# Kernel tuning notes

Hardware: AMD Instinct MI355X
Metric: run time of the kernel (lower is better)

The kernel has to match this reference:

```python
import jax, jax.numpy as jnp
import numpy as np

KERNEL = 128
STRIDE = 64


def setup_inputs() -> dict:
    key = jax.random.key(0)
    k1, k2, k3 = jax.random.split(key, 3)
    in_features = 8192
    fold_num = (in_features - KERNEL) // STRIDE + 1  # 127
    local_features = 128
    batch = 2048
    x = jax.random.normal(k1, (batch, in_features), dtype=jnp.float32)
    # stacked per-window Linear weights/biases (PyTorch Linear: y = x @ W.T + b)
    bound = 1.0 / np.sqrt(KERNEL)
    W = jax.random.uniform(k2, (fold_num, local_features, KERNEL), dtype=jnp.float32,
                           minval=-bound, maxval=bound)
    b = jax.random.uniform(k3, (fold_num, local_features), dtype=jnp.float32,
                           minval=-bound, maxval=bound)
    return {"x": x, "W": W, "b": b}


def reference(x, W, b):
    fold_num = W.shape[0]
    # window gather indices: [fold_num, kernel]
    idx = STRIDE * jnp.arange(fold_num)[:, None] + jnp.arange(KERNEL)[None, :]
    windows = x[:, idx]                      # [batch, fold_num, kernel]
    # per-window linear: out[b,f,l] = sum_k windows[b,f,k] * W[f,l,k] + b[f,l]
    out = jnp.einsum('bfk,flk->bfl', windows, W) + b[None, :, :]
    # concat along feature dim as in torch.cat(..., 1)
    return out.reshape(out.shape[0], -1)     # [batch, fold_num*local_features]
```

## Files before the change

kernel.cpp:

```cpp
#include <hip/hip_runtime.h>
#include <hip/hip_bf16.h>

typedef float f32x4 __attribute__((ext_vector_type(4)));
typedef __bf16 bf16x8 __attribute__((ext_vector_type(8)));

#define INF   8192
#define FOLDS 127
#define LOCAL 128
#define OUTF  (FOLDS * LOCAL)
#define BM    128

#define WB_BYTES ((size_t)FOLDS * LOCAL * 128 * 2)

__global__ void convert_w_kernel(const float* __restrict__ W, __bf16* __restrict__ Wb) {
    const size_t i = ((size_t)blockIdx.x * 256 + threadIdx.x) * 8;
    f32x4 v0 = *(const f32x4*)(W + i);
    f32x4 v1 = *(const f32x4*)(W + i + 4);
    bf16x8 w;
    w[0] = (__bf16)v0[0]; w[1] = (__bf16)v0[1]; w[2] = (__bf16)v0[2]; w[3] = (__bf16)v0[3];
    w[4] = (__bf16)v1[0]; w[5] = (__bf16)v1[1]; w[6] = (__bf16)v1[2]; w[7] = (__bf16)v1[3];
    *(bf16x8*)(Wb + i) = w;
}

__device__ __forceinline__ void cvt_store8(char* lds, int byte, f32x4 v0, f32x4 v1) {
    bf16x8 w;
    w[0] = (__bf16)v0[0]; w[1] = (__bf16)v0[1]; w[2] = (__bf16)v0[2]; w[3] = (__bf16)v0[3];
    w[4] = (__bf16)v1[0]; w[5] = (__bf16)v1[1]; w[6] = (__bf16)v1[2]; w[7] = (__bf16)v1[3];
    *(bf16x8*)(lds + byte) = w;
}

template<bool WBF16>
__global__ __launch_bounds__(256, 2)
void local_linear_kernel(const float* __restrict__ x,
                         const float* __restrict__ Wf32,
                         const __bf16* __restrict__ Wbf,
                         const float* __restrict__ bias,
                         float* __restrict__ out)
{
    __shared__ __align__(16) __bf16 As[128 * 192];
    __shared__ __align__(16) __bf16 Bs[128 * 128];

    const int mt = blockIdx.x;
    const int fg = blockIdx.y;
    const int f0 = fg * 2;
    const bool has_f1 = (f0 + 1) < FOLDS;
    const int t  = threadIdx.x;

    const int m0 = mt * BM;
    const float* __restrict__ xg = x + (size_t)m0 * INF + (size_t)f0 * 64;

    const int lane = t & 63;
    const int wid  = t >> 6;
    const int wm   = wid >> 1;
    const int wn   = wid & 1;
    const int r16  = lane & 15;
    const int kq   = lane >> 4;

    auto stageB = [&](int f) {
        if constexpr (WBF16) {
            const char* Wsrc = (const char*)(Wbf + (size_t)f * LOCAL * 128);
            #pragma unroll
            for (int c = 0; c < 8; ++c) {
                const int base  = wid * 8192 + c * 1024;
                const int b     = base + lane * 16;
                const int row   = b >> 8;
                const int inner = b & 255;
                const int srcb  = row * 256 + (inner ^ ((row & 7) << 4));
                __builtin_amdgcn_global_load_lds(
                    (const __attribute__((address_space(1))) void*)(Wsrc + srcb),
                    (__attribute__((address_space(3))) void*)((char*)Bs + base),
                    16, 0, 0);
            }
        } else {
            const float* Wf = Wf32 + (size_t)f * LOCAL * 128;
            #pragma unroll
            for (int it = 0; it < 8; ++it) {
                const int e = it * 2048 + t * 8;
                const int row = e >> 7, col = e & 127;
                const float* g = Wf + row * 128 + col;
                f32x4 v0 = *(const f32x4*)g;
                f32x4 v1 = *(const f32x4*)(g + 4);
                cvt_store8((char*)Bs, (row * 256 + col * 2) ^ ((row & 7) << 4), v0, v1);
            }
        }
    };

    stageB(f0);

    #pragma unroll
    for (int it = 0; it < 8; ++it) {
        const int e = it * 2048 + t * 8;
        const int row = e >> 7, col = e & 127;
        const float* g = xg + (size_t)row * INF + col;
        f32x4 v0 = *(const f32x4*)g;
        f32x4 v1 = *(const f32x4*)(g + 4);
        cvt_store8((char*)As, (row * 384 + col * 2) ^ ((row & 7) << 4), v0, v1);
    }
    if (has_f1) {
        #pragma unroll
        for (int it = 0; it < 4; ++it) {
            const int e = it * 2048 + t * 8;
            const int row = e >> 6, col = 128 + (e & 63);
            const float* g = xg + (size_t)row * INF + col;
            f32x4 v0 = *(const f32x4*)g;
            f32x4 v1 = *(const f32x4*)(g + 4);
            cvt_store8((char*)As, (row * 384 + col * 2) ^ ((row & 7) << 4), v0, v1);
        }
    }

    auto computeFold = [&](int f, int acolBase) {
        f32x4 acc[4][4];
        #pragma unroll
        for (int i = 0; i < 4; ++i)
            #pragma unroll
            for (int j = 0; j < 4; ++j)
                acc[i][j] = (f32x4){0.f, 0.f, 0.f, 0.f};

        #pragma unroll
        for (int ks = 0; ks < 4; ++ks) {
            const int kof = ks * 32 + kq * 8;
            bf16x8 a[4], b[4];
            #pragma unroll
            for (int i = 0; i < 4; ++i) {
                const int row  = wm * 64 + i * 16 + r16;
                const int byte = (row * 384 + (acolBase + kof) * 2) ^ ((row & 7) << 4);
                a[i] = *(const bf16x8*)((const char*)As + byte);
            }
            #pragma unroll
            for (int j = 0; j < 4; ++j) {
                const int row  = wn * 64 + j * 16 + r16;
                const int byte = (row * 256 + kof * 2) ^ ((row & 7) << 4);
                b[j] = *(const bf16x8*)((const char*)Bs + byte);
            }
            #pragma unroll
            for (int i = 0; i < 4; ++i)
                #pragma unroll
                for (int j = 0; j < 4; ++j)
                    acc[i][j] = __builtin_amdgcn_mfma_f32_16x16x32_bf16(a[i], b[j], acc[i][j], 0, 0, 0);
        }

        float bv[4];
        #pragma unroll
        for (int j = 0; j < 4; ++j)
            bv[j] = bias[f * LOCAL + wn * 64 + j * 16 + r16];

        #pragma unroll
        for (int i = 0; i < 4; ++i) {
            const int mrow = m0 + wm * 64 + i * 16 + kq * 4;
            #pragma unroll
            for (int j = 0; j < 4; ++j) {
                const int ncol = f * LOCAL + wn * 64 + j * 16 + r16;
                float* o = out + (size_t)mrow * OUTF + ncol;
                #pragma unroll
                for (int r = 0; r < 4; ++r)
                    o[(size_t)r * OUTF] = acc[i][j][r] + bv[j];
            }
        }
    };

    __syncthreads();
    computeFold(f0, 0);

    if (has_f1) {
        __syncthreads();
        stageB(f0 + 1);
        __syncthreads();
        computeFold(f0 + 1, 64);
    }
}

extern "C" void kernel_launch(void* const* d_in, const int* in_sizes, int n_in,
                              void* d_out, int out_size, void* d_ws, size_t ws_size,
                              hipStream_t stream) {
    const float* x    = (const float*)d_in[0];
    const float* W    = (const float*)d_in[1];
    const float* bias = (const float*)d_in[2];
    float* out        = (float*)d_out;

    dim3 grid(2048 / BM, 64);
    dim3 block(256);

    if (ws_size >= WB_BYTES) {
        __bf16* Wb = (__bf16*)d_ws;
        convert_w_kernel<<<1016, 256, 0, stream>>>(W, Wb);
        local_linear_kernel<true><<<grid, block, 0, stream>>>(x, W, Wb, bias, out);
    } else {
        local_linear_kernel<false><<<grid, block, 0, stream>>>(x, W, nullptr, bias, out);
    }
}
```

Before: 50.06 us.

## Assign one fold per block with 512 threads and nontemporal output stores

Each block now handles a single fold instead of two folds sequentially, with 8 waves splitting the 128x128 output tile into 4x2 wave tiles. The grid grows to 16x127 blocks. The bias is folded into the accumulator initialisation, and output stores become nontemporal. This removes the serial second-fold stage and its extra barriers and raises parallelism and occupancy. In exchange, the overlapping x window is loaded twice (once per adjacent fold) instead of being shared between the two folds of a block.

```diff
diff --git a/kernel.cpp b/kernel.cpp
--- a/kernel.cpp
+++ b/kernel.cpp
@@ -30,142 +30,113 @@
 }
 
 template<bool WBF16>
-__global__ __launch_bounds__(256, 2)
+__global__ __launch_bounds__(512, 4)
 void local_linear_kernel(const float* __restrict__ x,
                          const float* __restrict__ Wf32,
                          const __bf16* __restrict__ Wbf,
                          const float* __restrict__ bias,
                          float* __restrict__ out)
 {
-    __shared__ __align__(16) __bf16 As[128 * 192];
+    __shared__ __align__(16) __bf16 As[128 * 128];
     __shared__ __align__(16) __bf16 Bs[128 * 128];
 
     const int mt = blockIdx.x;
-    const int fg = blockIdx.y;
-    const int f0 = fg * 2;
-    const bool has_f1 = (f0 + 1) < FOLDS;
+    const int f  = blockIdx.y;
     const int t  = threadIdx.x;
 
-    const int m0 = mt * BM;
-    const float* __restrict__ xg = x + (size_t)m0 * INF + (size_t)f0 * 64;
-
+    const int m0   = mt * BM;
     const int lane = t & 63;
     const int wid  = t >> 6;
-    const int wm   = wid >> 1;
-    const int wn   = wid & 1;
+    const int wm   = wid >> 2;
+    const int wn   = wid & 3;
     const int r16  = lane & 15;
     const int kq   = lane >> 4;
 
-    auto stageB = [&](int f) {
-        if constexpr (WBF16) {
-            const char* Wsrc = (const char*)(Wbf + (size_t)f * LOCAL * 128);
-            #pragma unroll
-            for (int c = 0; c < 8; ++c) {
-                const int base  = wid * 8192 + c * 1024;
-                const int b     = base + lane * 16;
-                const int row   = b >> 8;
-                const int inner = b & 255;
-                const int srcb  = row * 256 + (inner ^ ((row & 7) << 4));
-                __builtin_amdgcn_global_load_lds(
-                    (const __attribute__((address_space(1))) void*)(Wsrc + srcb),
-                    (__attribute__((address_space(3))) void*)((char*)Bs + base),
-                    16, 0, 0);
-            }
-        } else {
-            const float* Wf = Wf32 + (size_t)f * LOCAL * 128;
-            #pragma unroll
-            for (int it = 0; it < 8; ++it) {
-                const int e = it * 2048 + t * 8;
-                const int row = e >> 7, col = e & 127;
-                const float* g = Wf + row * 128 + col;
-                f32x4 v0 = *(const f32x4*)g;
-                f32x4 v1 = *(const f32x4*)(g + 4);
-                cvt_store8((char*)Bs, (row * 256 + col * 2) ^ ((row & 7) << 4), v0, v1);
-            }
+    if constexpr (WBF16) {
+        const char* Wsrc = (const char*)(Wbf + (size_t)f * LOCAL * 128);
+        #pragma unroll
+        for (int c = 0; c < 4; ++c) {
+            const int base  = wid * 4096 + c * 1024;
+            const int b     = base + lane * 16;
+            const int row   = b >> 8;
+            const int inner = b & 255;
+            const int srcb  = row * 256 + (inner ^ ((row & 7) << 4));
+            __builtin_amdgcn_global_load_lds(
+                (const __attribute__((address_space(1))) void*)(Wsrc + srcb),
+                (__attribute__((address_space(3))) void*)((char*)Bs + base),
+                16, 0, 0);
         }
-    };
+    } else {
+        const float* Wf = Wf32 + (size_t)f * LOCAL * 128;
+        #pragma unroll
+        for (int it = 0; it < 4; ++it) {
+            const int e = it * 4096 + t * 8;
+            const int row = e >> 7, col = e & 127;
+            const float* g = Wf + row * 128 + col;
+            f32x4 v0 = *(const f32x4*)g;
+            f32x4 v1 = *(const f32x4*)(g + 4);
+            cvt_store8((char*)Bs, (row * 256 + col * 2) ^ ((row & 7) << 4), v0, v1);
+        }
+    }
 
-    stageB(f0);
-
+    const float* __restrict__ xg = x + (size_t)m0 * INF + (size_t)f * 64;
     #pragma unroll
-    for (int it = 0; it < 8; ++it) {
-        const int e = it * 2048 + t * 8;
+    for (int it = 0; it < 4; ++it) {
+        const int e = it * 4096 + t * 8;
         const int row = e >> 7, col = e & 127;
         const float* g = xg + (size_t)row * INF + col;
         f32x4 v0 = *(const f32x4*)g;
         f32x4 v1 = *(const f32x4*)(g + 4);
-        cvt_store8((char*)As, (row * 384 + col * 2) ^ ((row & 7) << 4), v0, v1);
+        cvt_store8((char*)As, (row * 256 + col * 2) ^ ((row & 7) << 4), v0, v1);
     }
-    if (has_f1) {
+    __syncthreads();
+
+    float bv[2];
+    #pragma unroll
+    for (int j = 0; j < 2; ++j)
+        bv[j] = bias[f * LOCAL + wn * 32 + j * 16 + r16];
+
+    f32x4 acc[4][2];
+    #pragma unroll
+    for (int i = 0; i < 4; ++i)
         #pragma unroll
-        for (int it = 0; it < 4; ++it) {
-            const int e = it * 2048 + t * 8;
-            const int row = e >> 6, col = 128 + (e & 63);
-            const float* g = xg + (size_t)row * INF + col;
-            f32x4 v0 = *(const f32x4*)g;
-            f32x4 v1 = *(const f32x4*)(g + 4);
-            cvt_store8((char*)As, (row * 384 + col * 2) ^ ((row & 7) << 4), v0, v1);
+        for (int j = 0; j < 2; ++j)
+            acc[i][j] = (f32x4){bv[j], bv[j], bv[j], bv[j]};
+
+    #pragma unroll
+    for (int ks = 0; ks < 4; ++ks) {
+        const int kof = ks * 32 + kq * 8;
+        bf16x8 a[4], b[2];
+        #pragma unroll
+        for (int i = 0; i < 4; ++i) {
+            const int row  = wm * 64 + i * 16 + r16;
+            const int byte = (row * 256 + kof * 2) ^ ((row & 7) << 4);
+            a[i] = *(const bf16x8*)((const char*)As + byte);
         }
-    }
-
-    auto computeFold = [&](int f, int acolBase) {
-        f32x4 acc[4][4];
+        #pragma unroll
+        for (int j = 0; j < 2; ++j) {
+            const int row  = wn * 32 + j * 16 + r16;
+            const int byte = (row * 256 + kof * 2) ^ ((row & 7) << 4);
+            b[j] = *(const bf16x8*)((const char*)Bs + byte);
+        }
         #pragma unroll
         for (int i = 0; i < 4; ++i)
             #pragma unroll
-            for (int j = 0; j < 4; ++j)
-                acc[i][j] = (f32x4){0.f, 0.f, 0.f, 0.f};
+            for (int j = 0; j < 2; ++j)
+                acc[i][j] = __builtin_amdgcn_mfma_f32_16x16x32_bf16(a[i], b[j], acc[i][j], 0, 0, 0);
+    }
 
+    #pragma unroll
+    for (int i = 0; i < 4; ++i) {
+        const int mrow = m0 + wm * 64 + i * 16 + kq * 4;
         #pragma unroll
-        for (int ks = 0; ks < 4; ++ks) {
-            const int kof = ks * 32 + kq * 8;
-            bf16x8 a[4], b[4];
+        for (int j = 0; j < 2; ++j) {
+            const int ncol = f * LOCAL + wn * 32 + j * 16 + r16;
+            float* o = out + (size_t)mrow * OUTF + ncol;
             #pragma unroll
-            for (int i = 0; i < 4; ++i) {
-                const int row  = wm * 64 + i * 16 + r16;
-                const int byte = (row * 384 + (acolBase + kof) * 2) ^ ((row & 7) << 4);
-                a[i] = *(const bf16x8*)((const char*)As + byte);
-            }
-            #pragma unroll
-            for (int j = 0; j < 4; ++j) {
-                const int row  = wn * 64 + j * 16 + r16;
-                const int byte = (row * 256 + kof * 2) ^ ((row & 7) << 4);
-                b[j] = *(const bf16x8*)((const char*)Bs + byte);
-            }
-            #pragma unroll
-            for (int i = 0; i < 4; ++i)
-                #pragma unroll
-                for (int j = 0; j < 4; ++j)
-                    acc[i][j] = __builtin_amdgcn_mfma_f32_16x16x32_bf16(a[i], b[j], acc[i][j], 0, 0, 0);
+            for (int r = 0; r < 4; ++r)
+                __builtin_nontemporal_store(acc[i][j][r], o + (size_t)r * OUTF);
         }
-
-        float bv[4];
-        #pragma unroll
-        for (int j = 0; j < 4; ++j)
-            bv[j] = bias[f * LOCAL + wn * 64 + j * 16 + r16];
-
-        #pragma unroll
-        for (int i = 0; i < 4; ++i) {
-            const int mrow = m0 + wm * 64 + i * 16 + kq * 4;
-            #pragma unroll
-            for (int j = 0; j < 4; ++j) {
-                const int ncol = f * LOCAL + wn * 64 + j * 16 + r16;
-                float* o = out + (size_t)mrow * OUTF + ncol;
-                #pragma unroll
-                for (int r = 0; r < 4; ++r)
-                    o[(size_t)r * OUTF] = acc[i][j][r] + bv[j];
-            }
-        }
-    };
-
-    __syncthreads();
-    computeFold(f0, 0);
-
-    if (has_f1) {
-        __syncthreads();
-        stageB(f0 + 1);
-        __syncthreads();
-        computeFold(f0 + 1, 64);
     }
 }
 
@@ -177,8 +148,8 @@
     const float* bias = (const float*)d_in[2];
     float* out        = (float*)d_out;
 
-    dim3 grid(2048 / BM, 64);
-    dim3 block(256);
+    dim3 grid(2048 / BM, FOLDS);
+    dim3 block(512);
 
     if (ws_size >= WB_BYTES) {
         __bf16* Wb = (__bf16*)d_ws;
```

After: 58.87 us. 1.18x slower.
